# Performance work log

Hardware: AMD Instinct MI355X
Metric: run time of the kernel (lower is better)

The kernel has to match this reference:

```python
import jax, jax.numpy as jnp
import numpy as np

NUM_USERS = 100_000
NUM_ITEMS = 50_000
N = NUM_USERS + NUM_ITEMS
DIM = 64
HOP = 3
NNZ = 3_200_000
BATCH = 4096


def setup_inputs() -> dict:
    key = jax.random.key(0)
    k = jax.random.split(key, 8)
    edge_row = jax.random.randint(k[0], (NNZ,), 0, N, dtype=jnp.int32)
    edge_col = jax.random.randint(k[1], (NNZ,), 0, N, dtype=jnp.int32)
    # normalized-Laplacian-like small positive values (~1/deg)
    edge_val = jax.random.uniform(k[2], (NNZ,), dtype=jnp.float32) * 0.05
    # xavier_normal-ish init for embedding tables
    std = (2.0 / (NUM_USERS + DIM)) ** 0.5
    user_emb = jax.random.normal(k[3], (NUM_USERS, DIM), dtype=jnp.float32) * 0.1
    item_emb = jax.random.normal(k[4], (NUM_ITEMS, DIM), dtype=jnp.float32) * 0.1
    users = jax.random.randint(k[5], (BATCH,), 0, NUM_USERS, dtype=jnp.int32)
    items = jax.random.randint(k[6], (BATCH,), 0, NUM_ITEMS, dtype=jnp.int32)
    negatives = jax.random.randint(k[7], (BATCH,), 0, NUM_ITEMS, dtype=jnp.int32)
    return {"edge_row": edge_row, "edge_col": edge_col, "edge_val": edge_val,
            "user_emb": user_emb, "item_emb": item_emb,
            "users": users, "items": items, "negatives": negatives}


def _spmm(edge_row, edge_col, edge_val, x):
    # y[r] = sum_e val[e] * x[col[e]]  (COO SpMM)
    msgs = edge_val[:, None] * x[edge_col]          # [nnz, d]
    return jax.ops.segment_sum(msgs, edge_row, num_segments=N)


def reference(edge_row, edge_col, edge_val, user_emb, item_emb, users, items, negatives):
    all_emb = jnp.concatenate((user_emb, item_emb), axis=0)   # [N, d]
    acc = all_emb
    x = all_emb
    for _ in range(HOP):
        x = _spmm(edge_row, edge_col, edge_val, x)
        acc = acc + x
    light_out = acc / jnp.float32(HOP + 1)                     # mean over hop+1 layers
    all_users_emb = light_out[:NUM_USERS]
    all_items_emb = light_out[NUM_USERS:]
    users_emb = all_users_emb[users]                           # [B, d]
    items_emb = all_items_emb[items]                           # [B, d]
    neg_item_emb = all_items_emb[negatives]                    # [B, d]
    pos_scores = jnp.sum(users_emb * items_emb, axis=1)
    neg_scores = jnp.sum(users_emb * neg_item_emb, axis=1)
    bpr_loss = jnp.mean(jax.nn.softplus(neg_scores - pos_scores))
    return bpr_loss
```

## Files before the change

kernel.cpp:

```cpp
#include <hip/hip_runtime.h>
#include <hip/hip_bf16.h>
#include <math.h>

#define NUM_USERS 100000
#define NUM_ITEMS 50000
#define N_NODES   (NUM_USERS + NUM_ITEMS)
#define DIM       64
#define NNZ_      3200000
#define BATCH_    4096

#define RPB     128
#define COLMASK 0x3FFFF

#define SB_ROWS 2048
#define NSB     74
#define NBUCK2  16
#define NRB     (NSB * NBUCK2)

#define P1_EPB  4096
#define P1_BLOCKS ((NNZ_ + P1_EPB - 1) / P1_EPB)
#define P2_EPB  4096
#define P2B     14
#define SBCAP   (P2B * P2_EPB)
#define BCAP    3584
#define PBCAP   (BCAP + RPB * 7)

#define VAL_SCALE  327680.0f
#define VAL_INV    (0.05f / 16384.0f)

typedef __attribute__((ext_vector_type(2))) float f32x2;


__device__ __forceinline__ unsigned pk4_fp8(float a, float b, float c, float d) {
    int w = __builtin_amdgcn_cvt_pk_fp8_f32(a, b, 0, false);
    w     = __builtin_amdgcn_cvt_pk_fp8_f32(c, d, w, true);
    return (unsigned)w;
}
__device__ __forceinline__ float dec8(unsigned byte) {
    return __builtin_amdgcn_cvt_f32_fp8((int)byte, 0);
}


__global__ void init_cursors(int* __restrict__ cursor1, int* __restrict__ cursor2) {
    int i = blockIdx.x * 256 + threadIdx.x;
    if (i < NSB) cursor1[i] = i * SBCAP;
    if (i < NRB) cursor2[i] = i * BCAP;
}


__global__ void part1(const int* __restrict__ erow, const int* __restrict__ ecol,
                      const float* __restrict__ eval_, int* __restrict__ cursor1,
                      int2* __restrict__ cpairs1) {
    __shared__ int h[NSB];
    __shared__ int bs[NSB];
    int t = threadIdx.x;
    int start = blockIdx.x * P1_EPB;
    int end = start + P1_EPB; if (end > NNZ_) end = NNZ_;

    if (t < NSB) h[t] = 0;
    __syncthreads();
    for (int i = start + t; i < end; i += 256)
        atomicAdd(&h[erow[i] >> 11], 1);
    __syncthreads();
    if (t < NSB) { int c = h[t]; bs[t] = c ? atomicAdd(&cursor1[t], c) : 0; }
    __syncthreads();
    if (t < NSB) h[t] = 0;
    __syncthreads();

    for (int i0 = start + t; i0 < end; i0 += 1024) {
        int r[4], c[4]; float v[4];
        #pragma unroll
        for (int k = 0; k < 4; ++k) {
            int idx = i0 + k * 256;
            if (idx < end) { r[k] = erow[idx]; c[k] = ecol[idx]; v[k] = eval_[idx]; }
            else r[k] = -1;
        }
        #pragma unroll
        for (int k = 0; k < 4; ++k) {
            if (r[k] >= 0) {
                int sb = r[k] >> 11;
                int pos = bs[sb] + atomicAdd(&h[sb], 1);
                cpairs1[pos] = make_int2(((r[k] & (SB_ROWS - 1)) << 18) | c[k],
                                         __float_as_int(v[k]));
            }
        }
    }
}


__global__ void part2(const int* __restrict__ cursor1, const int2* __restrict__ cpairs1,
                      int* __restrict__ cursor2, int2* __restrict__ cpairs2) {
    __shared__ int h[NBUCK2];
    __shared__ int bs[NBUCK2];
    int t = threadIdx.x;
    int sb = blockIdx.x / P2B, slice = blockIdx.x % P2B;
    int segEnd = cursor1[sb];
    int start = sb * SBCAP + slice * P2_EPB;
    int end = start + P2_EPB; if (end > segEnd) end = segEnd;

    if (t < NBUCK2) h[t] = 0;
    __syncthreads();
    for (int i = start + t; i < end; i += 256)
        atomicAdd(&h[cpairs1[i].x >> 25], 1);
    __syncthreads();
    if (t < NBUCK2) { int c = h[t]; bs[t] = c ? atomicAdd(&cursor2[sb * NBUCK2 + t], c) : 0; }
    __syncthreads();
    if (t < NBUCK2) h[t] = 0;
    __syncthreads();

    for (int i0 = start + t; i0 < end; i0 += 1024) {
        int2 p[4];
        #pragma unroll
        for (int k = 0; k < 4; ++k) {
            int idx = i0 + k * 256;
            p[k] = (idx < end) ? cpairs1[idx] : make_int2(-1, 0);
        }
        #pragma unroll
        for (int k = 0; k < 4; ++k) {
            if (p[k].x >= 0) {
                int b = p[k].x >> 25;
                int pos = bs[b] + atomicAdd(&h[b], 1);
                cpairs2[pos] = p[k];
            }
        }
    }
}


#define REF_THREADS 512

__global__ void refine(const int* __restrict__ cursor2, const int2* __restrict__ cpairs2,
                       int* __restrict__ rowptrP, int* __restrict__ rowendP,
                       unsigned* __restrict__ pairs) {
    __shared__ int hist[RPB];
    __shared__ int curs[RPB];
    __shared__ int offs[RPB];
    int t = threadIdx.x;
    int rb = blockIdx.x;
    int beg = rb * BCAP;
    int end = cursor2[rb];
    int pbase = rb * PBCAP;

    if (t < RPB) hist[t] = 0;
    __syncthreads();
    for (int i = beg + t; i < end; i += REF_THREADS)
        atomicAdd(&hist[(cpairs2[i].x >> 18) & (RPB - 1)], 1);
    __syncthreads();
    int pc = 0;
    if (t < RPB) { pc = (hist[t] + 7) & ~7; curs[t] = pc; }
    __syncthreads();
    for (int off = 1; off < RPB; off <<= 1) {
        int v = (t < RPB && t >= off) ? curs[t - off] : 0;
        __syncthreads();
        if (t < RPB) curs[t] += v;
        __syncthreads();
    }
    if (t < RPB) {
        int pex = curs[t] - pc;
        offs[t] = pex;
        int row = (rb >> 4) * SB_ROWS + (rb & (NBUCK2 - 1)) * RPB + t;
        if (row < N_NODES) {
            rowptrP[row] = pbase + pex;
            rowendP[row] = pbase + pex + pc;
        }
    }
    __syncthreads();
    if (t < RPB) curs[t] = 0;
    __syncthreads();
    for (int i = beg + t; i < end; i += REF_THREADS) {
        int2 p = cpairs2[i];
        int rl = (p.x >> 18) & (RPB - 1);
        int pos = pbase + offs[rl] + atomicAdd(&curs[rl], 1);
        unsigned vfix = (unsigned)fminf(__int_as_float(p.y) * VAL_SCALE + 0.5f, 16383.0f);
        pairs[pos] = ((unsigned)(p.x & COLMASK) << 14) | vfix;
    }
    __syncthreads();
    if (t < RPB) {
        int c = hist[t];
        int pcc = (c + 7) & ~7;
        int base2 = pbase + offs[t];
        for (int j = c; j < pcc; ++j) pairs[base2 + j] = 0u;
    }
}


__global__ void cvt_fp8(const float* __restrict__ ue, const float* __restrict__ ie,
                        unsigned* __restrict__ ef8) {
    int i = blockIdx.x * blockDim.x + threadIdx.x;
    const int NQ = N_NODES * DIM / 4;
    if (i >= NQ) return;
    const int UQ = NUM_USERS * DIM / 4;
    float4 v = (i < UQ) ? ((const float4*)ue)[i] : ((const float4*)ie)[i - UQ];
    ef8[i] = pk4_fp8(v.x, v.y, v.z, v.w);
}


__global__ void spmm_csr(const int* __restrict__ rowptrP, const int* __restrict__ rowendP,
                         const unsigned* __restrict__ pairs,
                         const unsigned char* __restrict__ x, unsigned char* __restrict__ out) {
    int w    = (blockIdx.x * blockDim.x + threadIdx.x) >> 6;
    int lane = threadIdx.x & 63;
    if (w >= N_NODES) return;
    int q   = lane >> 4;
    int sub = lane & 15;
    int beg = rowptrP[w], end = rowendP[w];

    float a0 = 0.f, a1 = 0.f, a2 = 0.f, a3 = 0.f;
    float b0 = 0.f, b1 = 0.f, b2 = 0.f, b3 = 0.f;

    int base = beg + q;
    if ((end - beg) & 8) {
        unsigned pA = pairs[base];
        unsigned pB = pairs[base + 4];
        unsigned vA = *(const unsigned*)(x + (size_t)(pA >> 14) * DIM + 4 * sub);
        unsigned vB = *(const unsigned*)(x + (size_t)(pB >> 14) * DIM + 4 * sub);
        float sA = (float)(pA & 0x3FFFu) * VAL_INV;
        float sB = (float)(pB & 0x3FFFu) * VAL_INV;
        f32x2 loA = __builtin_amdgcn_cvt_pk_f32_fp8((int)vA, false);
        f32x2 hiA = __builtin_amdgcn_cvt_pk_f32_fp8((int)vA, true);
        f32x2 loB = __builtin_amdgcn_cvt_pk_f32_fp8((int)vB, false);
        f32x2 hiB = __builtin_amdgcn_cvt_pk_f32_fp8((int)vB, true);
        a0 = fmaf(sA, loA.x, a0); a1 = fmaf(sA, loA.y, a1);
        a2 = fmaf(sA, hiA.x, a2); a3 = fmaf(sA, hiA.y, a3);
        b0 = fmaf(sB, loB.x, b0); b1 = fmaf(sB, loB.y, b1);
        b2 = fmaf(sB, hiB.x, b2); b3 = fmaf(sB, hiB.y, b3);
        base += 8;
    }
    for (; base < end; base += 16) {
        unsigned p0 = pairs[base];
        unsigned p1 = pairs[base + 4];
        unsigned p2 = pairs[base + 8];
        unsigned p3 = pairs[base + 12];
        unsigned v0 = *(const unsigned*)(x + (size_t)(p0 >> 14) * DIM + 4 * sub);
        unsigned v1 = *(const unsigned*)(x + (size_t)(p1 >> 14) * DIM + 4 * sub);
        unsigned v2 = *(const unsigned*)(x + (size_t)(p2 >> 14) * DIM + 4 * sub);
        unsigned v3 = *(const unsigned*)(x + (size_t)(p3 >> 14) * DIM + 4 * sub);
        float s0 = (float)(p0 & 0x3FFFu) * VAL_INV;
        float s1 = (float)(p1 & 0x3FFFu) * VAL_INV;
        float s2 = (float)(p2 & 0x3FFFu) * VAL_INV;
        float s3 = (float)(p3 & 0x3FFFu) * VAL_INV;
        f32x2 lo0 = __builtin_amdgcn_cvt_pk_f32_fp8((int)v0, false);
        f32x2 hi0 = __builtin_amdgcn_cvt_pk_f32_fp8((int)v0, true);
        f32x2 lo1 = __builtin_amdgcn_cvt_pk_f32_fp8((int)v1, false);
        f32x2 hi1 = __builtin_amdgcn_cvt_pk_f32_fp8((int)v1, true);
        f32x2 lo2 = __builtin_amdgcn_cvt_pk_f32_fp8((int)v2, false);
        f32x2 hi2 = __builtin_amdgcn_cvt_pk_f32_fp8((int)v2, true);
        f32x2 lo3 = __builtin_amdgcn_cvt_pk_f32_fp8((int)v3, false);
        f32x2 hi3 = __builtin_amdgcn_cvt_pk_f32_fp8((int)v3, true);
        a0 = fmaf(s0, lo0.x, a0); a1 = fmaf(s0, lo0.y, a1);
        a2 = fmaf(s0, hi0.x, a2); a3 = fmaf(s0, hi0.y, a3);
        b0 = fmaf(s1, lo1.x, b0); b1 = fmaf(s1, lo1.y, b1);
        b2 = fmaf(s1, hi1.x, b2); b3 = fmaf(s1, hi1.y, b3);
        a0 = fmaf(s2, lo2.x, a0); a1 = fmaf(s2, lo2.y, a1);
        a2 = fmaf(s2, hi2.x, a2); a3 = fmaf(s2, hi2.y, a3);
        b0 = fmaf(s3, lo3.x, b0); b1 = fmaf(s3, lo3.y, b1);
        b2 = fmaf(s3, hi3.x, b2); b3 = fmaf(s3, hi3.y, b3);
    }
    a0 += b0; a1 += b1; a2 += b2; a3 += b3;

    a0 += __shfl_xor(a0, 16); a0 += __shfl_xor(a0, 32);
    a1 += __shfl_xor(a1, 16); a1 += __shfl_xor(a1, 32);
    a2 += __shfl_xor(a2, 16); a2 += __shfl_xor(a2, 32);
    a3 += __shfl_xor(a3, 16); a3 += __shfl_xor(a3, 32);

    if (lane < 16) {
        *(unsigned*)(out + (size_t)w * DIM + 4 * sub) = pk4_fp8(a0, a1, a2, a3);
    }
}


__device__ __forceinline__ float emb0(const float* __restrict__ ue,
                                      const float* __restrict__ ie,
                                      int node, int lane) {
    return (node < NUM_USERS) ? ue[(size_t)node * DIM + lane]
                              : ie[(size_t)(node - NUM_USERS) * DIM + lane];
}

__device__ __forceinline__ float hop3(const int* __restrict__ rowptrP,
                                      const int* __restrict__ rowendP,
                                      const unsigned* __restrict__ pairs,
                                      const unsigned char* __restrict__ h2, int node, int lane) {
    int beg = rowptrP[node], end = rowendP[node];
    float a0 = 0.f, a1 = 0.f, a2 = 0.f, a3 = 0.f;
    for (int base = beg; base < end; base += 8) {
        unsigned p[8];
        #pragma unroll
        for (int k = 0; k < 8; ++k) p[k] = pairs[base + k];
        float xv[8];
        #pragma unroll
        for (int k = 0; k < 8; ++k)
            xv[k] = dec8(h2[(size_t)(p[k] >> 14) * DIM + lane]);
        a0 = fmaf((float)(p[0] & 0x3FFFu) * VAL_INV, xv[0], a0);
        a1 = fmaf((float)(p[1] & 0x3FFFu) * VAL_INV, xv[1], a1);
        a2 = fmaf((float)(p[2] & 0x3FFFu) * VAL_INV, xv[2], a2);
        a3 = fmaf((float)(p[3] & 0x3FFFu) * VAL_INV, xv[3], a3);
        a0 = fmaf((float)(p[4] & 0x3FFFu) * VAL_INV, xv[4], a0);
        a1 = fmaf((float)(p[5] & 0x3FFFu) * VAL_INV, xv[5], a1);
        a2 = fmaf((float)(p[6] & 0x3FFFu) * VAL_INV, xv[6], a2);
        a3 = fmaf((float)(p[7] & 0x3FFFu) * VAL_INV, xv[7], a3);
    }
    return (a0 + a1) + (a2 + a3);
}

__global__ void score_fused(const float* __restrict__ ue, const float* __restrict__ ie,
                            const unsigned char* __restrict__ h1,
                            const unsigned char* __restrict__ h2,
                            const int* __restrict__ rowptrP, const int* __restrict__ rowendP,
                            const unsigned* __restrict__ pairs,
                            const int* __restrict__ users, const int* __restrict__ items,
                            const int* __restrict__ negs,
                            float* __restrict__ out) {
    __shared__ float vecs[3][DIM];
    int b    = blockIdx.x;
    int role = threadIdx.x >> 6;
    int lane = threadIdx.x & 63;

    int node = (role == 0) ? users[b]
             : (role == 1) ? NUM_USERS + items[b]
                           : NUM_USERS + negs[b];

    size_t o = (size_t)node * DIM + lane;
    float v = emb0(ue, ie, node, lane) + dec8(h1[o]) + dec8(h2[o]) +
              hop3(rowptrP, rowendP, pairs, h2, node, lane);
    vecs[role][lane] = v;
    __syncthreads();

    if (role == 0) {
        float u   = v;
        float pos = u * vecs[1][lane];
        float neg = u * vecs[2][lane];
        #pragma unroll
        for (int s = 32; s >= 1; s >>= 1) {
            pos += __shfl_xor(pos, s);
            neg += __shfl_xor(neg, s);
        }
        if (lane == 0) {
            float x = (neg - pos) * (1.0f / 16.0f);
            float sp = fmaxf(x, 0.0f) + log1pf(expf(-fabsf(x)));
            atomicAdd(out, sp * (1.0f / BATCH_));
        }
    }
}


extern "C" void kernel_launch(void* const* d_in, const int* in_sizes, int n_in,
                              void* d_out, int out_size, void* d_ws, size_t ws_size,
                              hipStream_t stream) {
    const int*   edge_row  = (const int*)d_in[0];
    const int*   edge_col  = (const int*)d_in[1];
    const float* edge_val  = (const float*)d_in[2];
    const float* user_emb  = (const float*)d_in[3];
    const float* item_emb  = (const float*)d_in[4];
    const int*   users     = (const int*)d_in[5];
    const int*   items     = (const int*)d_in[6];
    const int*   negatives = (const int*)d_in[7];
    float* out = (float*)d_out;

    int* w = (int*)d_ws;
    int*  cursor1 = w;
    int*  cursor2 = cursor1 + NSB;
    int*  rowptrP = cursor2 + NRB;
    int*  rowendP = rowptrP + N_NODES;
    int2*     cpairs1 = (int2*)(rowendP + N_NODES);
    int2*     cpairs2 = cpairs1 + (size_t)NSB * SBCAP;
    unsigned* pairs   = (unsigned*)cpairs1;
    unsigned* ef8     = (unsigned*)(cpairs2 + (size_t)NSB * SBCAP);
    unsigned* h1w     = ef8 + (size_t)N_NODES * DIM / 4;
    unsigned* h2w     = h1w + (size_t)N_NODES * DIM / 4;

    hipMemsetAsync(d_out, 0, sizeof(float), stream);

    const int blk = 256;
    const int cvtBlocks = (N_NODES * DIM / 4 + blk - 1) / blk;
    const int rowWaveBlocks = (N_NODES * 64 + blk - 1) / blk;

    init_cursors<<<(NRB + 255) / 256, blk, 0, stream>>>(cursor1, cursor2);
    part1<<<P1_BLOCKS, blk, 0, stream>>>(edge_row, edge_col, edge_val, cursor1, cpairs1);
    part2<<<NSB * P2B, blk, 0, stream>>>(cursor1, cpairs1, cursor2, cpairs2);
    refine<<<NRB, REF_THREADS, 0, stream>>>(cursor2, cpairs2, rowptrP, rowendP, pairs);
    cvt_fp8<<<cvtBlocks, blk, 0, stream>>>(user_emb, item_emb, ef8);

    spmm_csr<<<rowWaveBlocks, blk, 0, stream>>>(rowptrP, rowendP, pairs,
                                                (const unsigned char*)ef8, (unsigned char*)h1w);
    spmm_csr<<<rowWaveBlocks, blk, 0, stream>>>(rowptrP, rowendP, pairs,
                                                (const unsigned char*)h1w, (unsigned char*)h2w);

    score_fused<<<BATCH_, 192, 0, stream>>>(user_emb, item_emb,
                                            (const unsigned char*)h1w,
                                            (const unsigned char*)h2w,
                                            rowptrP, rowendP, pairs,
                                            users, items, negatives, out);
}
```

Before: 271.5 us.

## Replace two-level row bucketing with single per-superblock counting sort

Shrinks the first-pass bucket to 1024 rows (147 buckets) and replaces the part2 and refine kernels with one kernel, sort_sb. Each of its 1024-thread blocks does a per-row counting sort over a whole superblock directly from cpairs1. This removes one full scatter pass over the edge list and one kernel launch. The cost is only 147 blocks of parallelism, which may underuse the GPU, and a larger shared-memory histogram and prefix-scan per block.

```diff
diff --git a/kernel.cpp b/kernel.cpp
--- a/kernel.cpp
+++ b/kernel.cpp
@@ -9,21 +9,15 @@
 #define NNZ_      3200000
 #define BATCH_    4096
 
-#define RPB     128
 #define COLMASK 0x3FFFF
 
-#define SB_ROWS 2048
-#define NSB     74
-#define NBUCK2  16
-#define NRB     (NSB * NBUCK2)
+#define SB_ROWS 1024
+#define NSB     147
+#define SBCAP   24576
+#define PBCAP   (SBCAP + SB_ROWS * 7)
 
 #define P1_EPB  4096
 #define P1_BLOCKS ((NNZ_ + P1_EPB - 1) / P1_EPB)
-#define P2_EPB  4096
-#define P2B     14
-#define SBCAP   (P2B * P2_EPB)
-#define BCAP    3584
-#define PBCAP   (BCAP + RPB * 7)
 
 #define VAL_SCALE  327680.0f
 #define VAL_INV    (0.05f / 16384.0f)
@@ -41,10 +35,9 @@
 }
 
 
-__global__ void init_cursors(int* __restrict__ cursor1, int* __restrict__ cursor2) {
+__global__ void init_cursors(int* __restrict__ cursor1) {
     int i = blockIdx.x * 256 + threadIdx.x;
     if (i < NSB) cursor1[i] = i * SBCAP;
-    if (i < NRB) cursor2[i] = i * BCAP;
 }
 
 
@@ -60,7 +53,7 @@
     if (t < NSB) h[t] = 0;
     __syncthreads();
     for (int i = start + t; i < end; i += 256)
-        atomicAdd(&h[erow[i] >> 11], 1);
+        atomicAdd(&h[erow[i] >> 10], 1);
     __syncthreads();
     if (t < NSB) { int c = h[t]; bs[t] = c ? atomicAdd(&cursor1[t], c) : 0; }
     __syncthreads();
@@ -78,7 +71,7 @@
         #pragma unroll
         for (int k = 0; k < 4; ++k) {
             if (r[k] >= 0) {
-                int sb = r[k] >> 11;
+                int sb = r[k] >> 10;
                 int pos = bs[sb] + atomicAdd(&h[sb], 1);
                 cpairs1[pos] = make_int2(((r[k] & (SB_ROWS - 1)) << 18) | c[k],
                                          __float_as_int(v[k]));
@@ -88,98 +81,59 @@
 }
 
 
-__global__ void part2(const int* __restrict__ cursor1, const int2* __restrict__ cpairs1,
-                      int* __restrict__ cursor2, int2* __restrict__ cpairs2) {
-    __shared__ int h[NBUCK2];
-    __shared__ int bs[NBUCK2];
+#define SORT_THREADS 1024
+
+__global__ void sort_sb(const int* __restrict__ cursor1, const int2* __restrict__ cpairs1,
+                        int* __restrict__ rowptrP, int* __restrict__ rowendP,
+                        unsigned* __restrict__ pairs) {
+    __shared__ int hist[SB_ROWS];
+    __shared__ int offs[SB_ROWS];
+    __shared__ int curs[SB_ROWS];
     int t = threadIdx.x;
-    int sb = blockIdx.x / P2B, slice = blockIdx.x % P2B;
-    int segEnd = cursor1[sb];
-    int start = sb * SBCAP + slice * P2_EPB;
-    int end = start + P2_EPB; if (end > segEnd) end = segEnd;
-
-    if (t < NBUCK2) h[t] = 0;
-    __syncthreads();
-    for (int i = start + t; i < end; i += 256)
-        atomicAdd(&h[cpairs1[i].x >> 25], 1);
-    __syncthreads();
-    if (t < NBUCK2) { int c = h[t]; bs[t] = c ? atomicAdd(&cursor2[sb * NBUCK2 + t], c) : 0; }
-    __syncthreads();
-    if (t < NBUCK2) h[t] = 0;
-    __syncthreads();
-
-    for (int i0 = start + t; i0 < end; i0 += 1024) {
-        int2 p[4];
-        #pragma unroll
-        for (int k = 0; k < 4; ++k) {
-            int idx = i0 + k * 256;
-            p[k] = (idx < end) ? cpairs1[idx] : make_int2(-1, 0);
-        }
-        #pragma unroll
-        for (int k = 0; k < 4; ++k) {
-            if (p[k].x >= 0) {
-                int b = p[k].x >> 25;
-                int pos = bs[b] + atomicAdd(&h[b], 1);
-                cpairs2[pos] = p[k];
-            }
-        }
-    }
-}
-
-
-#define REF_THREADS 512
-
-__global__ void refine(const int* __restrict__ cursor2, const int2* __restrict__ cpairs2,
-                       int* __restrict__ rowptrP, int* __restrict__ rowendP,
-                       unsigned* __restrict__ pairs) {
-    __shared__ int hist[RPB];
-    __shared__ int curs[RPB];
-    __shared__ int offs[RPB];
-    int t = threadIdx.x;
-    int rb = blockIdx.x;
-    int beg = rb * BCAP;
-    int end = cursor2[rb];
-    int pbase = rb * PBCAP;
-
-    if (t < RPB) hist[t] = 0;
-    __syncthreads();
-    for (int i = beg + t; i < end; i += REF_THREADS)
-        atomicAdd(&hist[(cpairs2[i].x >> 18) & (RPB - 1)], 1);
-    __syncthreads();
-    int pc = 0;
-    if (t < RPB) { pc = (hist[t] + 7) & ~7; curs[t] = pc; }
-    __syncthreads();
-    for (int off = 1; off < RPB; off <<= 1) {
-        int v = (t < RPB && t >= off) ? curs[t - off] : 0;
+    int sb = blockIdx.x;
+    int beg = sb * SBCAP;
+    int end = cursor1[sb];
+    int pbase = sb * PBCAP;
+
+    hist[t] = 0;
+    __syncthreads();
+    for (int i = beg + t; i < end; i += SORT_THREADS)
+        atomicAdd(&hist[(cpairs1[i].x >> 18) & (SB_ROWS - 1)], 1);
+    __syncthreads();
+    int pc = (hist[t] + 7) & ~7;
+    curs[t] = pc;
+    __syncthreads();
+    for (int off = 1; off < SB_ROWS; off <<= 1) {
+        int v = (t >= off) ? curs[t - off] : 0;
         __syncthreads();
-        if (t < RPB) curs[t] += v;
+        curs[t] += v;
         __syncthreads();
     }
-    if (t < RPB) {
-        int pex = curs[t] - pc;
-        offs[t] = pex;
-        int row = (rb >> 4) * SB_ROWS + (rb & (NBUCK2 - 1)) * RPB + t;
+    int pex = curs[t] - pc;
+    offs[t] = pex;
+    {
+        int row = sb * SB_ROWS + t;
         if (row < N_NODES) {
             rowptrP[row] = pbase + pex;
             rowendP[row] = pbase + pex + pc;
         }
     }
     __syncthreads();
-    if (t < RPB) curs[t] = 0;
-    __syncthreads();
-    for (int i = beg + t; i < end; i += REF_THREADS) {
-        int2 p = cpairs2[i];
-        int rl = (p.x >> 18) & (RPB - 1);
+    curs[t] = 0;
+    __syncthreads();
+    for (int i = beg + t; i < end; i += SORT_THREADS) {
+        int2 p = cpairs1[i];
+        int rl = (p.x >> 18) & (SB_ROWS - 1);
         int pos = pbase + offs[rl] + atomicAdd(&curs[rl], 1);
         unsigned vfix = (unsigned)fminf(__int_as_float(p.y) * VAL_SCALE + 0.5f, 16383.0f);
         pairs[pos] = ((unsigned)(p.x & COLMASK) << 14) | vfix;
     }
     __syncthreads();
-    if (t < RPB) {
+    {
         int c = hist[t];
         int pcc = (c + 7) & ~7;
-        int base2 = pbase + offs[t];
-        for (int j = c; j < pcc; ++j) pairs[base2 + j] = 0u;
+        int b2 = pbase + offs[t];
+        for (int j = c; j < pcc; ++j) pairs[b2 + j] = 0u;
     }
 }
 
@@ -358,13 +312,11 @@
 
     int* w = (int*)d_ws;
     int*  cursor1 = w;
-    int*  cursor2 = cursor1 + NSB;
-    int*  rowptrP = cursor2 + NRB;
+    int*  rowptrP = cursor1 + NSB + 1;
     int*  rowendP = rowptrP + N_NODES;
     int2*     cpairs1 = (int2*)(rowendP + N_NODES);
-    int2*     cpairs2 = cpairs1 + (size_t)NSB * SBCAP;
-    unsigned* pairs   = (unsigned*)cpairs1;
-    unsigned* ef8     = (unsigned*)(cpairs2 + (size_t)NSB * SBCAP);
+    unsigned* pairs   = (unsigned*)(cpairs1 + (size_t)NSB * SBCAP);
+    unsigned* ef8     = pairs + (size_t)NSB * PBCAP;
     unsigned* h1w     = ef8 + (size_t)N_NODES * DIM / 4;
     unsigned* h2w     = h1w + (size_t)N_NODES * DIM / 4;
 
@@ -374,10 +326,9 @@
     const int cvtBlocks = (N_NODES * DIM / 4 + blk - 1) / blk;
     const int rowWaveBlocks = (N_NODES * 64 + blk - 1) / blk;
 
-    init_cursors<<<(NRB + 255) / 256, blk, 0, stream>>>(cursor1, cursor2);
+    init_cursors<<<1, blk, 0, stream>>>(cursor1);
     part1<<<P1_BLOCKS, blk, 0, stream>>>(edge_row, edge_col, edge_val, cursor1, cpairs1);
-    part2<<<NSB * P2B, blk, 0, stream>>>(cursor1, cpairs1, cursor2, cpairs2);
-    refine<<<NRB, REF_THREADS, 0, stream>>>(cursor2, cpairs2, rowptrP, rowendP, pairs);
+    sort_sb<<<NSB, SORT_THREADS, 0, stream>>>(cursor1, cpairs1, rowptrP, rowendP, pairs);
     cvt_fp8<<<cvtBlocks, blk, 0, stream>>>(user_emb, item_emb, ef8);
 
     spmm_csr<<<rowWaveBlocks, blk, 0, stream>>>(rowptrP, rowendP, pairs,
```

New measurement: 276.1 us. About the same (+1.7%).
